# Performance work log

Hardware: AMD Instinct MI355X
Metric: run time of the kernel (lower is better)

Reference implementation:

```python
import jax, jax.numpy as jnp
import numpy as np

C_IN, C, N_HEAD = 256, 32, 8

def setup_inputs() -> dict:
    key = jax.random.key(0)
    ks = jax.random.split(key, 9)
    B, S = 4, 2048
    x = jax.random.normal(ks[0], (B, S, C_IN), dtype=jnp.float32)
    bias = jax.random.normal(ks[1], (1, N_HEAD, S, S), dtype=jnp.float32)
    s = 0.02
    Wq = jax.random.normal(ks[2], (C_IN, C * N_HEAD), dtype=jnp.float32) * s
    Wk = jax.random.normal(ks[3], (C_IN, C * N_HEAD), dtype=jnp.float32) * s
    Wv = jax.random.normal(ks[4], (C_IN, C * N_HEAD), dtype=jnp.float32) * s
    Wg = jax.random.normal(ks[5], (C_IN, C * N_HEAD), dtype=jnp.float32) * s
    bg = jnp.zeros((C * N_HEAD,), dtype=jnp.float32)
    Wo = jax.random.normal(ks[6], (C * N_HEAD, C_IN), dtype=jnp.float32) * s
    bo = jnp.zeros((C_IN,), dtype=jnp.float32)
    return {"x": x, "bias": bias, "Wq": Wq, "Wk": Wk, "Wv": Wv,
            "Wg": Wg, "bg": bg, "Wo": Wo, "bo": bo}

def reference(x, bias, Wq, Wk, Wv, Wg, bg, Wo, bo):
    B, S, _ = x.shape
    # projections (attn_dim = -2, so no movedim needed for [B, S, c_in])
    q = (x @ Wq).reshape(B, S, N_HEAD, C).transpose(0, 2, 1, 3)  # [B,H,S,C]
    k = (x @ Wk).reshape(B, S, N_HEAD, C).transpose(0, 2, 1, 3)
    v = (x @ Wv).reshape(B, S, N_HEAD, C).transpose(0, 2, 1, 3)
    q = q / jnp.sqrt(jnp.asarray(C, dtype=q.dtype))
    a = jnp.einsum('bhqc,bhkc->bhqk', q, k) + bias  # [B,H,S,S]
    a = jax.nn.softmax(a, axis=-1)
    o = jnp.einsum('bhqk,bhkc->bhqc', a, v)         # [B,H,S,C]
    o = o.transpose(0, 2, 1, 3).reshape(B, S, N_HEAD * C)
    g = jax.nn.sigmoid(x @ Wg + bg)
    o = g * o
    return o @ Wo + bo
```

## Files before the change

### kernel.cpp

```cpp
#include <hip/hip_runtime.h>

#define BB   4
#define SS   2048
#define HH   8
#define CC   32
#define CIN  256

typedef unsigned short u16;
typedef u16 u16x4 __attribute__((ext_vector_type(4)));
typedef u16 u16x8 __attribute__((ext_vector_type(8)));
typedef __bf16 bf16x8 __attribute__((ext_vector_type(8)));
typedef float f32x4 __attribute__((ext_vector_type(4)));

__device__ __forceinline__ f32x4 mfma16(u16x8 a, u16x8 b, f32x4 c) {
  return __builtin_amdgcn_mfma_f32_16x16x32_bf16(
      __builtin_bit_cast(bf16x8, a), __builtin_bit_cast(bf16x8, b), c, 0, 0, 0);
}

__device__ __forceinline__ u16 bf16_rne(float x) {
  unsigned u = __float_as_uint(x);
  u += 0x7FFFu + ((u >> 16) & 1u);
  return (u16)(u >> 16);
}
__device__ __forceinline__ void cvt_pair(float x, u16 &hi, u16 &lo) {
  hi = bf16_rne(x);
  lo = bf16_rne(x - __uint_as_float(((unsigned)hi) << 16));
}

__global__ void k_cvt_x(const float* __restrict__ x,
                        u16* __restrict__ xh, u16* __restrict__ xl) {
  int i = (blockIdx.x * 256 + threadIdx.x) * 4;
  float4 v = *(const float4*)(x + i);
  u16x4 h, l;
  u16 th, tl;
  cvt_pair(v.x, th, tl); h[0] = th; l[0] = tl;
  cvt_pair(v.y, th, tl); h[1] = th; l[1] = tl;
  cvt_pair(v.z, th, tl); h[2] = th; l[2] = tl;
  cvt_pair(v.w, th, tl); h[3] = th; l[3] = tl;
  *(u16x4*)(xh + i) = h;
  *(u16x4*)(xl + i) = l;
}

__global__ void k_cvt_w(const float* __restrict__ Wq, const float* __restrict__ Wk,
                        const float* __restrict__ Wv, const float* __restrict__ Wg,
                        const float* __restrict__ Wo,
                        u16* __restrict__ wt4h, u16* __restrict__ wt4l,
                        u16* __restrict__ woth, u16* __restrict__ wotl) {
  int nb = blockIdx.x, t = threadIdx.x;
  if (nb < 1024) {
    const float* W = (nb < 256) ? Wq : (nb < 512) ? Wk : (nb < 768) ? Wv : Wg;
    int n = nb & 255;
    u16 hi, lo; cvt_pair(W[t * 256 + n], hi, lo);
    wt4h[nb * 256 + t] = hi; wt4l[nb * 256 + t] = lo;
  } else {
    int n = nb - 1024;
    u16 hi, lo; cvt_pair(Wo[t * 256 + n], hi, lo);
    woth[n * 256 + t] = hi; wotl[n * 256 + t] = lo;
  }
}

__global__ __launch_bounds__(256, 2) void k_proj(
    const u16* __restrict__ xh, const u16* __restrict__ xl,
    const u16* __restrict__ wt4h, const u16* __restrict__ wt4l,
    const float* __restrict__ bg,
    u16* __restrict__ qh, u16* __restrict__ ql,
    u16* __restrict__ kh, u16* __restrict__ kl,
    u16* __restrict__ vth, u16* __restrict__ vtl,
    float* __restrict__ g) {
  const int m0 = blockIdx.x * 128;
  const int n0 = blockIdx.y * 128;
  const int wave = threadIdx.x >> 6;
  const int lane = threadIdx.x & 63;
  const int wm = (wave >> 1) * 64, wn = (wave & 1) * 64;
  const int l15 = lane & 15, lg = lane >> 4;

  f32x4 acc[4][4] = {};
  for (int ks = 0; ks < 8; ++ks) {
    u16x8 a_h[4], a_l[4], b_h[4], b_l[4];
#pragma unroll
    for (int mt = 0; mt < 4; ++mt) {
      int row = m0 + wm + mt * 16 + l15;
      int base = row * 256 + ks * 32 + lg * 8;
      a_h[mt] = *(const u16x8*)(xh + base);
      a_l[mt] = *(const u16x8*)(xl + base);
    }
#pragma unroll
    for (int nt = 0; nt < 4; ++nt) {
      int col = n0 + wn + nt * 16 + l15;
      int base = col * 256 + ks * 32 + lg * 8;
      b_h[nt] = *(const u16x8*)(wt4h + base);
      b_l[nt] = *(const u16x8*)(wt4l + base);
    }
#pragma unroll
    for (int mt = 0; mt < 4; ++mt)
#pragma unroll
      for (int nt = 0; nt < 4; ++nt) {
        acc[mt][nt] = mfma16(a_h[mt], b_h[nt], acc[mt][nt]);
        acc[mt][nt] = mfma16(a_h[mt], b_l[nt], acc[mt][nt]);
        acc[mt][nt] = mfma16(a_l[mt], b_h[nt], acc[mt][nt]);
      }
  }

  const float qscale = 0.17677669529663687f;
#pragma unroll
  for (int mt = 0; mt < 4; ++mt)
#pragma unroll
    for (int nt = 0; nt < 4; ++nt)
#pragma unroll
      for (int r = 0; r < 4; ++r) {
        int row = m0 + wm + mt * 16 + lg * 4 + r;
        int col = n0 + wn + nt * 16 + l15;
        float val = acc[mt][nt][r];
        int b = row >> 11, s = row & 2047;
        int mid = col >> 8, d = col & 255;
        int h = d >> 5, c = d & 31;
        if (mid == 3) {
          float gv = 1.0f / (1.0f + __expf(-(val + bg[d])));
          g[row * 256 + d] = gv;
        } else if (mid == 2) {
          u16 hi, lo; cvt_pair(val, hi, lo);
          int idx = ((b * HH + h) * CC + c) * SS + s;
          vth[idx] = hi; vtl[idx] = lo;
        } else {
          if (mid == 0) val *= qscale;
          u16 hi, lo; cvt_pair(val, hi, lo);
          int idx = ((b * HH + h) * SS + s) * CC + c;
          if (mid == 0) { qh[idx] = hi; ql[idx] = lo; }
          else          { kh[idx] = hi; kl[idx] = lo; }
        }
      }
}

__global__ __launch_bounds__(256, 2) void k_attn(
    const u16* __restrict__ qh, const u16* __restrict__ ql,
    const u16* __restrict__ kh, const u16* __restrict__ kl,
    const u16* __restrict__ vth, const u16* __restrict__ vtl,
    const float* __restrict__ bias, float* __restrict__ o) {
  __shared__ u16 ph[4][32][72];
  __shared__ u16 pl[4][32][72];
  const int h = blockIdx.y;
  const int q0 = blockIdx.x * 32;
  const int wave = threadIdx.x >> 6;
  const int b = wave;
  const int lane = threadIdx.x & 63;
  const int l15 = lane & 15, lg = lane >> 4;
  const int bh = b * HH + h;

  u16x8 qfh[2], qfl[2];
#pragma unroll
  for (int mt = 0; mt < 2; ++mt) {
    int base = (bh * SS + q0 + mt * 16 + l15) * CC + lg * 8;
    qfh[mt] = *(const u16x8*)(qh + base);
    qfl[mt] = *(const u16x8*)(ql + base);
  }

  f32x4 oacc[2][2] = {};
  float rs[2][4] = {};
  const float* biasH = bias + h * SS * SS;

  for (int jt = 0; jt < 32; ++jt) {
    const int j0 = jt * 64;
    float bv[2][4][4];
#pragma unroll
    for (int mt = 0; mt < 2; ++mt)
#pragma unroll
      for (int r = 0; r < 4; ++r) {
        const float* bp = biasH + (q0 + mt * 16 + lg * 4 + r) * SS + j0 + l15;
#pragma unroll
        for (int nt = 0; nt < 4; ++nt) bv[mt][nt][r] = bp[nt * 16];
      }
    u16x8 kf_h[4], kf_l[4];
#pragma unroll
    for (int nt = 0; nt < 4; ++nt) {
      int base = (bh * SS + j0 + nt * 16 + l15) * CC + lg * 8;
      kf_h[nt] = *(const u16x8*)(kh + base);
      kf_l[nt] = *(const u16x8*)(kl + base);
    }
    f32x4 sacc[2][4];
#pragma unroll
    for (int mt = 0; mt < 2; ++mt)
#pragma unroll
      for (int nt = 0; nt < 4; ++nt) {
        f32x4 z = {0.0f, 0.0f, 0.0f, 0.0f};
        z = mfma16(qfh[mt], kf_h[nt], z);
        z = mfma16(qfh[mt], kf_l[nt], z);
        z = mfma16(qfl[mt], kf_h[nt], z);
        sacc[mt][nt] = z;
      }
#pragma unroll
    for (int mt = 0; mt < 2; ++mt)
#pragma unroll
      for (int nt = 0; nt < 4; ++nt)
#pragma unroll
        for (int r = 0; r < 4; ++r) {
          float xv = sacc[mt][nt][r] + bv[mt][nt][r];
          float p = __expf(xv);
          rs[mt][r] += p;
          u16 hi, lo; cvt_pair(p, hi, lo);
          int q = mt * 16 + lg * 4 + r;
          int j = nt * 16 + l15;
          ph[wave][q][j] = hi;
          pl[wave][q][j] = lo;
        }
#pragma unroll
    for (int ks = 0; ks < 2; ++ks) {
      u16x8 pah[2], pal[2];
#pragma unroll
      for (int mt = 0; mt < 2; ++mt) {
        pah[mt] = *(const u16x8*)&ph[wave][mt * 16 + l15][ks * 32 + lg * 8];
        pal[mt] = *(const u16x8*)&pl[wave][mt * 16 + l15][ks * 32 + lg * 8];
      }
#pragma unroll
      for (int ct = 0; ct < 2; ++ct) {
        int base = (bh * CC + ct * 16 + l15) * SS + j0 + ks * 32 + lg * 8;
        u16x8 vfh = *(const u16x8*)(vth + base);
        u16x8 vfl = *(const u16x8*)(vtl + base);
#pragma unroll
        for (int mt = 0; mt < 2; ++mt) {
          oacc[mt][ct] = mfma16(pah[mt], vfh, oacc[mt][ct]);
          oacc[mt][ct] = mfma16(pah[mt], vfl, oacc[mt][ct]);
          oacc[mt][ct] = mfma16(pal[mt], vfh, oacc[mt][ct]);
        }
      }
    }
  }

#pragma unroll
  for (int mt = 0; mt < 2; ++mt)
#pragma unroll
    for (int r = 0; r < 4; ++r) {
      float v = rs[mt][r];
      v += __shfl_xor(v, 1, 64);
      v += __shfl_xor(v, 2, 64);
      v += __shfl_xor(v, 4, 64);
      v += __shfl_xor(v, 8, 64);
      rs[mt][r] = v;
    }
#pragma unroll
  for (int mt = 0; mt < 2; ++mt)
#pragma unroll
    for (int ct = 0; ct < 2; ++ct)
#pragma unroll
      for (int r = 0; r < 4; ++r) {
        int qrow = q0 + mt * 16 + lg * 4 + r;
        int c = ct * 16 + l15;
        o[((b * SS + qrow) * HH + h) * CC + c] = oacc[mt][ct][r] / rs[mt][r];
      }
}

__global__ __launch_bounds__(256, 2) void k_out(
    const float* __restrict__ o, const float* __restrict__ g,
    const u16* __restrict__ woth, const u16* __restrict__ wotl,
    const float* __restrict__ bo, float* __restrict__ out) {
  const int m0 = blockIdx.x * 128;
  const int n0 = blockIdx.y * 128;
  const int wave = threadIdx.x >> 6;
  const int lane = threadIdx.x & 63;
  const int wm = (wave >> 1) * 64, wn = (wave & 1) * 64;
  const int l15 = lane & 15, lg = lane >> 4;

  f32x4 acc[4][4] = {};
  for (int ks = 0; ks < 8; ++ks) {
    u16x8 a_h[4], a_l[4], b_h[4], b_l[4];
#pragma unroll
    for (int mt = 0; mt < 4; ++mt) {
      int base = (m0 + wm + mt * 16 + l15) * 256 + ks * 32 + lg * 8;
      float4 o0 = *(const float4*)(o + base);
      float4 o1 = *(const float4*)(o + base + 4);
      float4 g0 = *(const float4*)(g + base);
      float4 g1 = *(const float4*)(g + base + 4);
      float pr[8] = {o0.x * g0.x, o0.y * g0.y, o0.z * g0.z, o0.w * g0.w,
                     o1.x * g1.x, o1.y * g1.y, o1.z * g1.z, o1.w * g1.w};
      union { u16 s[8]; u16x8 v; } uh, ul;
#pragma unroll
      for (int e = 0; e < 8; ++e) { u16 th, tl; cvt_pair(pr[e], th, tl); uh.s[e] = th; ul.s[e] = tl; }
      a_h[mt] = uh.v; a_l[mt] = ul.v;
    }
#pragma unroll
    for (int nt = 0; nt < 4; ++nt) {
      int base = (n0 + wn + nt * 16 + l15) * 256 + ks * 32 + lg * 8;
      b_h[nt] = *(const u16x8*)(woth + base);
      b_l[nt] = *(const u16x8*)(wotl + base);
    }
#pragma unroll
    for (int mt = 0; mt < 4; ++mt)
#pragma unroll
      for (int nt = 0; nt < 4; ++nt) {
        acc[mt][nt] = mfma16(a_h[mt], b_h[nt], acc[mt][nt]);
        acc[mt][nt] = mfma16(a_h[mt], b_l[nt], acc[mt][nt]);
        acc[mt][nt] = mfma16(a_l[mt], b_h[nt], acc[mt][nt]);
      }
  }
#pragma unroll
  for (int mt = 0; mt < 4; ++mt)
#pragma unroll
    for (int nt = 0; nt < 4; ++nt)
#pragma unroll
      for (int r = 0; r < 4; ++r) {
        int row = m0 + wm + mt * 16 + lg * 4 + r;
        int col = n0 + wn + nt * 16 + l15;
        out[row * 256 + col] = acc[mt][nt][r] + bo[col];
      }
}

extern "C" void kernel_launch(void* const* d_in, const int* in_sizes, int n_in,
                              void* d_out, int out_size, void* d_ws, size_t ws_size,
                              hipStream_t stream) {
  const float* x    = (const float*)d_in[0];
  const float* bias = (const float*)d_in[1];
  const float* Wq   = (const float*)d_in[2];
  const float* Wk   = (const float*)d_in[3];
  const float* Wv   = (const float*)d_in[4];
  const float* Wg   = (const float*)d_in[5];
  const float* bg   = (const float*)d_in[6];
  const float* Wo   = (const float*)d_in[7];
  const float* bo   = (const float*)d_in[8];
  float* out = (float*)d_out;

  char* p = (char*)d_ws;
  size_t used = 0;
  auto alloc = [&](size_t bytes) -> void* {
    void* r = p + used;
    used += (bytes + 255) & ~(size_t)255;
    return r;
  };
  const size_t NTOK = (size_t)BB * SS * CIN;
  u16* xh   = (u16*)alloc(NTOK * 2);
  u16* xl   = (u16*)alloc(NTOK * 2);
  u16* wt4h = (u16*)alloc(1024 * 256 * 2);
  u16* wt4l = (u16*)alloc(1024 * 256 * 2);
  u16* woth = (u16*)alloc(256 * 256 * 2);
  u16* wotl = (u16*)alloc(256 * 256 * 2);
  u16* qh   = (u16*)alloc(NTOK * 2);
  u16* ql   = (u16*)alloc(NTOK * 2);
  u16* kh   = (u16*)alloc(NTOK * 2);
  u16* kl   = (u16*)alloc(NTOK * 2);
  u16* vth  = (u16*)alloc(NTOK * 2);
  u16* vtl  = (u16*)alloc(NTOK * 2);
  float* gbuf = (float*)alloc(NTOK * 4);
  float* obuf = (float*)alloc(NTOK * 4);
  if (used > ws_size) return;

  k_cvt_x<<<dim3(2048), dim3(256), 0, stream>>>(x, xh, xl);
  k_cvt_w<<<dim3(1280), dim3(256), 0, stream>>>(Wq, Wk, Wv, Wg, Wo, wt4h, wt4l, woth, wotl);
  k_proj<<<dim3(64, 8), dim3(256), 0, stream>>>(xh, xl, wt4h, wt4l, bg,
                                                qh, ql, kh, kl, vth, vtl, gbuf);
  k_attn<<<dim3(64, 8), dim3(256), 0, stream>>>(qh, ql, kh, kl, vth, vtl, bias, obuf);
  k_out<<<dim3(64, 2), dim3(256), 0, stream>>>(obuf, gbuf, woth, wotl, bo, out);
}
```

Before: 198.5 us.

## Restructure attention to per-batch blocks with transposed scores, tile weight conversion

The attention kernel now assigns one batch and 64 queries per block, with each wave owning 16 query rows. It computes S^T = K·Q^T with the bias preloaded into the accumulator as contiguous float4 loads, and stages P through a swizzled u32 LDS tile. The weight conversion kernel uses a shared-memory transpose tile so its reads and writes are coalesced. The projection kernel writes V as vectorized u16x4, and the output GEMM uses smaller tiles to launch more blocks. The intent is to cut uncoalesced bias and weight traffic, reduce per-block register use and raise occupancy, at the cost of reloading K and V per batch block.

```diff
diff --git a/kernel.cpp b/kernel.cpp
--- a/kernel.cpp
+++ b/kernel.cpp
@@ -7,6 +7,7 @@
 #define CIN  256
 
 typedef unsigned short u16;
+typedef unsigned int   u32;
 typedef u16 u16x4 __attribute__((ext_vector_type(4)));
 typedef u16 u16x8 __attribute__((ext_vector_type(8)));
 typedef __bf16 bf16x8 __attribute__((ext_vector_type(8)));
@@ -46,16 +47,28 @@
                         const float* __restrict__ Wo,
                         u16* __restrict__ wt4h, u16* __restrict__ wt4l,
                         u16* __restrict__ woth, u16* __restrict__ wotl) {
-  int nb = blockIdx.x, t = threadIdx.x;
-  if (nb < 1024) {
-    const float* W = (nb < 256) ? Wq : (nb < 512) ? Wk : (nb < 768) ? Wv : Wg;
-    int n = nb & 255;
-    u16 hi, lo; cvt_pair(W[t * 256 + n], hi, lo);
-    wt4h[nb * 256 + t] = hi; wt4l[nb * 256 + t] = lo;
-  } else {
-    int n = nb - 1024;
-    u16 hi, lo; cvt_pair(Wo[t * 256 + n], hi, lo);
-    woth[n * 256 + t] = hi; wotl[n * 256 + t] = lo;
+  __shared__ float tile[64][65];
+  const int mat = blockIdx.x / 16, tt = blockIdx.x % 16;
+  const int m0 = (tt >> 2) * 64, n0 = (tt & 3) * 64;
+  const float* W = (mat == 0) ? Wq : (mat == 1) ? Wk : (mat == 2) ? Wv
+                 : (mat == 3) ? Wg : Wo;
+  const int tr = threadIdx.x >> 6;
+  const int tc = threadIdx.x & 63;
+#pragma unroll
+  for (int i = 0; i < 16; ++i) {
+    int row = i * 4 + tr;
+    tile[row][tc] = W[(m0 + row) * 256 + n0 + tc];
+  }
+  __syncthreads();
+  u16* dh = (mat < 4) ? wt4h : woth;
+  u16* dl = (mat < 4) ? wt4l : wotl;
+  const int nbase = (mat < 4) ? mat * 256 : 0;
+#pragma unroll
+  for (int i = 0; i < 16; ++i) {
+    int row = i * 4 + tr;
+    u16 hi, lo; cvt_pair(tile[tc][row], hi, lo);
+    dh[(nbase + n0 + row) * 256 + m0 + tc] = hi;
+    dl[(nbase + n0 + row) * 256 + m0 + tc] = lo;
   }
 }
 
@@ -79,15 +92,13 @@
     u16x8 a_h[4], a_l[4], b_h[4], b_l[4];
 #pragma unroll
     for (int mt = 0; mt < 4; ++mt) {
-      int row = m0 + wm + mt * 16 + l15;
-      int base = row * 256 + ks * 32 + lg * 8;
+      int base = (m0 + wm + mt * 16 + l15) * 256 + ks * 32 + lg * 8;
       a_h[mt] = *(const u16x8*)(xh + base);
       a_l[mt] = *(const u16x8*)(xl + base);
     }
 #pragma unroll
     for (int nt = 0; nt < 4; ++nt) {
-      int col = n0 + wn + nt * 16 + l15;
-      int base = col * 256 + ks * 32 + lg * 8;
+      int base = (n0 + wn + nt * 16 + l15) * 256 + ks * 32 + lg * 8;
       b_h[nt] = *(const u16x8*)(wt4h + base);
       b_l[nt] = *(const u16x8*)(wt4l + base);
     }
@@ -105,166 +116,162 @@
 #pragma unroll
   for (int mt = 0; mt < 4; ++mt)
 #pragma unroll
-    for (int nt = 0; nt < 4; ++nt)
-#pragma unroll
-      for (int r = 0; r < 4; ++r) {
-        int row = m0 + wm + mt * 16 + lg * 4 + r;
-        int col = n0 + wn + nt * 16 + l15;
-        float val = acc[mt][nt][r];
-        int b = row >> 11, s = row & 2047;
-        int mid = col >> 8, d = col & 255;
-        int h = d >> 5, c = d & 31;
-        if (mid == 3) {
-          float gv = 1.0f / (1.0f + __expf(-(val + bg[d])));
-          g[row * 256 + d] = gv;
-        } else if (mid == 2) {
-          u16 hi, lo; cvt_pair(val, hi, lo);
-          int idx = ((b * HH + h) * CC + c) * SS + s;
-          vth[idx] = hi; vtl[idx] = lo;
-        } else {
+    for (int nt = 0; nt < 4; ++nt) {
+      const int rowb = m0 + wm + mt * 16 + lg * 4;
+      const int col  = n0 + wn + nt * 16 + l15;
+      const int bb = rowb >> 11, s = rowb & 2047;
+      const int mid = col >> 8, d = col & 255;
+      const int hh = d >> 5, c = d & 31;
+      if (mid == 3) {
+#pragma unroll
+        for (int r = 0; r < 4; ++r) {
+          float gv = 1.0f / (1.0f + __expf(-(acc[mt][nt][r] + bg[d])));
+          g[(rowb + r) * 256 + d] = gv;
+        }
+      } else if (mid == 2) {
+        u16x4 vh4, vl4;
+#pragma unroll
+        for (int r = 0; r < 4; ++r) {
+          u16 th, tl; cvt_pair(acc[mt][nt][r], th, tl);
+          vh4[r] = th; vl4[r] = tl;
+        }
+        size_t idx = ((size_t)(bb * HH + hh) * CC + c) * SS + s;
+        *(u16x4*)(vth + idx) = vh4;
+        *(u16x4*)(vtl + idx) = vl4;
+      } else {
+#pragma unroll
+        for (int r = 0; r < 4; ++r) {
+          float val = acc[mt][nt][r];
           if (mid == 0) val *= qscale;
-          u16 hi, lo; cvt_pair(val, hi, lo);
-          int idx = ((b * HH + h) * SS + s) * CC + c;
-          if (mid == 0) { qh[idx] = hi; ql[idx] = lo; }
-          else          { kh[idx] = hi; kl[idx] = lo; }
+          u16 th, tl; cvt_pair(val, th, tl);
+          size_t idx = ((size_t)(bb * HH + hh) * SS + s + r) * CC + c;
+          if (mid == 0) { qh[idx] = th; ql[idx] = tl; }
+          else          { kh[idx] = th; kl[idx] = tl; }
         }
       }
-}
-
-__global__ __launch_bounds__(256, 2) void k_attn(
+    }
+}
+
+__global__ __launch_bounds__(256, 4) void k_attn(
     const u16* __restrict__ qh, const u16* __restrict__ ql,
     const u16* __restrict__ kh, const u16* __restrict__ kl,
     const u16* __restrict__ vth, const u16* __restrict__ vtl,
     const float* __restrict__ bias, float* __restrict__ o) {
-  __shared__ u16 ph[4][32][72];
-  __shared__ u16 pl[4][32][72];
-  const int h = blockIdx.y;
-  const int q0 = blockIdx.x * 32;
-  const int wave = threadIdx.x >> 6;
-  const int b = wave;
+  __shared__ __align__(16) u32 pth[4][16][32];
+  __shared__ __align__(16) u32 ptl[4][16][32];
+  const int idx = blockIdx.x;
+  const int h  = idx & 7;
+  const int t  = idx >> 3;
+  const int b  = t >> 5;
+  const int q0 = (t & 31) * 64;
+  const int w    = threadIdx.x >> 6;
   const int lane = threadIdx.x & 63;
   const int l15 = lane & 15, lg = lane >> 4;
   const int bh = b * HH + h;
-
-  u16x8 qfh[2], qfl[2];
-#pragma unroll
-  for (int mt = 0; mt < 2; ++mt) {
-    int base = (bh * SS + q0 + mt * 16 + l15) * CC + lg * 8;
-    qfh[mt] = *(const u16x8*)(qh + base);
-    qfl[mt] = *(const u16x8*)(ql + base);
-  }
-
-  f32x4 oacc[2][2] = {};
-  float rs[2][4] = {};
-  const float* biasH = bias + h * SS * SS;
-
+  const int qw = q0 + w * 16;
+  const int sw = (l15 & 7) << 2;
+
+  u16x8 qfh, qfl;
+  {
+    int base = (bh * SS + qw + l15) * CC + lg * 8;
+    qfh = *(const u16x8*)(qh + base);
+    qfl = *(const u16x8*)(ql + base);
+  }
+
+  f32x4 oacc[2] = {};
+  float rs = 0.0f;
+  const float* biasQ = bias + (size_t)h * SS * SS + (size_t)(qw + l15) * SS;
+
+#pragma unroll 1
   for (int jt = 0; jt < 32; ++jt) {
     const int j0 = jt * 64;
-    float bv[2][4][4];
-#pragma unroll
-    for (int mt = 0; mt < 2; ++mt)
-#pragma unroll
-      for (int r = 0; r < 4; ++r) {
-        const float* bp = biasH + (q0 + mt * 16 + lg * 4 + r) * SS + j0 + l15;
-#pragma unroll
-        for (int nt = 0; nt < 4; ++nt) bv[mt][nt][r] = bp[nt * 16];
-      }
-    u16x8 kf_h[4], kf_l[4];
-#pragma unroll
-    for (int nt = 0; nt < 4; ++nt) {
-      int base = (bh * SS + j0 + nt * 16 + l15) * CC + lg * 8;
-      kf_h[nt] = *(const u16x8*)(kh + base);
-      kf_l[nt] = *(const u16x8*)(kl + base);
-    }
-    f32x4 sacc[2][4];
-#pragma unroll
-    for (int mt = 0; mt < 2; ++mt)
-#pragma unroll
-      for (int nt = 0; nt < 4; ++nt) {
-        f32x4 z = {0.0f, 0.0f, 0.0f, 0.0f};
-        z = mfma16(qfh[mt], kf_h[nt], z);
-        z = mfma16(qfh[mt], kf_l[nt], z);
-        z = mfma16(qfl[mt], kf_h[nt], z);
-        sacc[mt][nt] = z;
-      }
-#pragma unroll
-    for (int mt = 0; mt < 2; ++mt)
-#pragma unroll
-      for (int nt = 0; nt < 4; ++nt)
-#pragma unroll
-        for (int r = 0; r < 4; ++r) {
-          float xv = sacc[mt][nt][r] + bv[mt][nt][r];
-          float p = __expf(xv);
-          rs[mt][r] += p;
-          u16 hi, lo; cvt_pair(p, hi, lo);
-          int q = mt * 16 + lg * 4 + r;
-          int j = nt * 16 + l15;
-          ph[wave][q][j] = hi;
-          pl[wave][q][j] = lo;
-        }
+    f32x4 sacc[4];
+#pragma unroll
+    for (int at = 0; at < 4; ++at) {
+      float4 bv = *(const float4*)(biasQ + j0 + at * 16 + lg * 4);
+      f32x4 z = {bv.x, bv.y, bv.z, bv.w};
+      sacc[at] = z;
+    }
+    u16x8 ka_h[4], ka_l[4];
+#pragma unroll
+    for (int at = 0; at < 4; ++at) {
+      int base = (bh * SS + j0 + at * 16 + l15) * CC + lg * 8;
+      ka_h[at] = *(const u16x8*)(kh + base);
+      ka_l[at] = *(const u16x8*)(kl + base);
+    }
+#pragma unroll
+    for (int at = 0; at < 4; ++at) {
+      sacc[at] = mfma16(ka_h[at], qfh, sacc[at]);
+      sacc[at] = mfma16(ka_h[at], qfl, sacc[at]);
+      sacc[at] = mfma16(ka_l[at], qfh, sacc[at]);
+    }
+#pragma unroll
+    for (int at = 0; at < 4; ++at) {
+      float p0 = __expf(sacc[at][0]);
+      float p1 = __expf(sacc[at][1]);
+      float p2 = __expf(sacc[at][2]);
+      float p3 = __expf(sacc[at][3]);
+      rs += (p0 + p1) + (p2 + p3);
+      u16 h0,l0,h1,l1,h2,l2,h3,l3;
+      cvt_pair(p0, h0, l0); cvt_pair(p1, h1, l1);
+      cvt_pair(p2, h2, l2); cvt_pair(p3, h3, l3);
+      uint2 Hv, Lv;
+      Hv.x = (u32)h0 | ((u32)h1 << 16);  Hv.y = (u32)h2 | ((u32)h3 << 16);
+      Lv.x = (u32)l0 | ((u32)l1 << 16);  Lv.y = (u32)l2 | ((u32)l3 << 16);
+      int col = (8 * at + 2 * lg) ^ sw;
+      *(uint2*)&pth[w][l15][col] = Hv;
+      *(uint2*)&ptl[w][l15][col] = Lv;
+    }
 #pragma unroll
     for (int ks = 0; ks < 2; ++ks) {
-      u16x8 pah[2], pal[2];
-#pragma unroll
-      for (int mt = 0; mt < 2; ++mt) {
-        pah[mt] = *(const u16x8*)&ph[wave][mt * 16 + l15][ks * 32 + lg * 8];
-        pal[mt] = *(const u16x8*)&pl[wave][mt * 16 + l15][ks * 32 + lg * 8];
-      }
+      int col = (ks * 16 + 4 * lg) ^ sw;
+      u16x8 pa_h = *(const u16x8*)&pth[w][l15][col];
+      u16x8 pa_l = *(const u16x8*)&ptl[w][l15][col];
 #pragma unroll
       for (int ct = 0; ct < 2; ++ct) {
         int base = (bh * CC + ct * 16 + l15) * SS + j0 + ks * 32 + lg * 8;
         u16x8 vfh = *(const u16x8*)(vth + base);
         u16x8 vfl = *(const u16x8*)(vtl + base);
-#pragma unroll
-        for (int mt = 0; mt < 2; ++mt) {
-          oacc[mt][ct] = mfma16(pah[mt], vfh, oacc[mt][ct]);
-          oacc[mt][ct] = mfma16(pah[mt], vfl, oacc[mt][ct]);
-          oacc[mt][ct] = mfma16(pal[mt], vfh, oacc[mt][ct]);
-        }
-      }
-    }
-  }
-
-#pragma unroll
-  for (int mt = 0; mt < 2; ++mt)
+        oacc[ct] = mfma16(pa_h, vfh, oacc[ct]);
+        oacc[ct] = mfma16(pa_h, vfl, oacc[ct]);
+        oacc[ct] = mfma16(pa_l, vfh, oacc[ct]);
+      }
+    }
+  }
+
+  rs += __shfl_xor(rs, 16, 64);
+  rs += __shfl_xor(rs, 32, 64);
+  float rsT[4];
+#pragma unroll
+  for (int r = 0; r < 4; ++r) rsT[r] = __shfl(rs, lg * 4 + r, 64);
+
+#pragma unroll
+  for (int ct = 0; ct < 2; ++ct)
 #pragma unroll
     for (int r = 0; r < 4; ++r) {
-      float v = rs[mt][r];
-      v += __shfl_xor(v, 1, 64);
-      v += __shfl_xor(v, 2, 64);
-      v += __shfl_xor(v, 4, 64);
-      v += __shfl_xor(v, 8, 64);
-      rs[mt][r] = v;
-    }
-#pragma unroll
-  for (int mt = 0; mt < 2; ++mt)
-#pragma unroll
-    for (int ct = 0; ct < 2; ++ct)
-#pragma unroll
-      for (int r = 0; r < 4; ++r) {
-        int qrow = q0 + mt * 16 + lg * 4 + r;
-        int c = ct * 16 + l15;
-        o[((b * SS + qrow) * HH + h) * CC + c] = oacc[mt][ct][r] / rs[mt][r];
-      }
+      int qg = qw + lg * 4 + r;
+      o[((size_t)(b * SS + qg) * HH + h) * CC + ct * 16 + l15] =
+          oacc[ct][r] / rsT[r];
+    }
 }
 
 __global__ __launch_bounds__(256, 2) void k_out(
     const float* __restrict__ o, const float* __restrict__ g,
     const u16* __restrict__ woth, const u16* __restrict__ wotl,
     const float* __restrict__ bo, float* __restrict__ out) {
-  const int m0 = blockIdx.x * 128;
+  const int m0 = blockIdx.x * 32;
   const int n0 = blockIdx.y * 128;
   const int wave = threadIdx.x >> 6;
   const int lane = threadIdx.x & 63;
-  const int wm = (wave >> 1) * 64, wn = (wave & 1) * 64;
+  const int wn = wave * 32;
   const int l15 = lane & 15, lg = lane >> 4;
 
-  f32x4 acc[4][4] = {};
+  f32x4 acc[2][2] = {};
   for (int ks = 0; ks < 8; ++ks) {
-    u16x8 a_h[4], a_l[4], b_h[4], b_l[4];
-#pragma unroll
-    for (int mt = 0; mt < 4; ++mt) {
-      int base = (m0 + wm + mt * 16 + l15) * 256 + ks * 32 + lg * 8;
+    u16x8 a_h[2], a_l[2], b_h[2], b_l[2];
+#pragma unroll
+    for (int mt = 0; mt < 2; ++mt) {
+      int base = (m0 + mt * 16 + l15) * 256 + ks * 32 + lg * 8;
       float4 o0 = *(const float4*)(o + base);
       float4 o1 = *(const float4*)(o + base + 4);
       float4 g0 = *(const float4*)(g + base);
@@ -277,27 +284,27 @@
       a_h[mt] = uh.v; a_l[mt] = ul.v;
     }
 #pragma unroll
-    for (int nt = 0; nt < 4; ++nt) {
+    for (int nt = 0; nt < 2; ++nt) {
       int base = (n0 + wn + nt * 16 + l15) * 256 + ks * 32 + lg * 8;
       b_h[nt] = *(const u16x8*)(woth + base);
       b_l[nt] = *(const u16x8*)(wotl + base);
     }
 #pragma unroll
-    for (int mt = 0; mt < 4; ++mt)
-#pragma unroll
-      for (int nt = 0; nt < 4; ++nt) {
+    for (int mt = 0; mt < 2; ++mt)
+#pragma unroll
+      for (int nt = 0; nt < 2; ++nt) {
         acc[mt][nt] = mfma16(a_h[mt], b_h[nt], acc[mt][nt]);
         acc[mt][nt] = mfma16(a_h[mt], b_l[nt], acc[mt][nt]);
         acc[mt][nt] = mfma16(a_l[mt], b_h[nt], acc[mt][nt]);
       }
   }
 #pragma unroll
-  for (int mt = 0; mt < 4; ++mt)
-#pragma unroll
-    for (int nt = 0; nt < 4; ++nt)
+  for (int mt = 0; mt < 2; ++mt)
+#pragma unroll
+    for (int nt = 0; nt < 2; ++nt)
 #pragma unroll
       for (int r = 0; r < 4; ++r) {
-        int row = m0 + wm + mt * 16 + lg * 4 + r;
+        int row = m0 + mt * 16 + lg * 4 + r;
         int col = n0 + wn + nt * 16 + l15;
         out[row * 256 + col] = acc[mt][nt][r] + bo[col];
       }
@@ -342,9 +349,9 @@
   if (used > ws_size) return;
 
   k_cvt_x<<<dim3(2048), dim3(256), 0, stream>>>(x, xh, xl);
-  k_cvt_w<<<dim3(1280), dim3(256), 0, stream>>>(Wq, Wk, Wv, Wg, Wo, wt4h, wt4l, woth, wotl);
+  k_cvt_w<<<dim3(80), dim3(256), 0, stream>>>(Wq, Wk, Wv, Wg, Wo, wt4h, wt4l, woth, wotl);
   k_proj<<<dim3(64, 8), dim3(256), 0, stream>>>(xh, xl, wt4h, wt4l, bg,
                                                 qh, ql, kh, kl, vth, vtl, gbuf);
-  k_attn<<<dim3(64, 8), dim3(256), 0, stream>>>(qh, ql, kh, kl, vth, vtl, bias, obuf);
-  k_out<<<dim3(64, 2), dim3(256), 0, stream>>>(obuf, gbuf, woth, wotl, bo, out);
-}
+  k_attn<<<dim3(1024), dim3(256), 0, stream>>>(qh, ql, kh, kl, vth, vtl, bias, obuf);
+  k_out<<<dim3(256, 2), dim3(256), 0, stream>>>(obuf, gbuf, woth, wotl, bo, out);
+}
```

After: 302.8 us. 1.52x slower.
